# Optimization experiments

Measured on AMD Instinct MI355X. Metric: run time of the kernel, lower is better.

Reference implementation:

```python
import jax, jax.numpy as jnp
import numpy as np

VOCAB, H, L, B, T = 32000, 256, 10, 256, 512


def setup_inputs() -> dict:
    key = jax.random.key(0)
    ks = jax.random.split(key, 6)
    s = 1.0 / np.sqrt(H)
    return {
        "tokens": jax.random.randint(ks[0], (B, T), 0, VOCAB),
        "hidden0": jnp.zeros((L, B, H), jnp.float32),
        "emb": jax.random.normal(ks[1], (VOCAB, H), jnp.float32),
        "Wx_w": jax.random.normal(ks[2], (L, H, H), jnp.float32) * s,
        "Wx_b": jax.random.normal(ks[3], (L, H), jnp.float32) * s,
        "Wh_w": jax.random.normal(ks[4], (L, H, H), jnp.float32) * s,
        "Wh_b": jax.random.normal(ks[5], (L, H), jnp.float32) * s,
    }


def reference(tokens, hidden0, emb, Wx_w, Wx_b, Wh_w, Wh_b):
    # tokens: [B,T] int; hidden0: [L,B,H]; weights stacked over layers.
    embedded = emb[tokens]                    # [B,T,H]
    xs = jnp.swapaxes(embedded, 0, 1)         # [T,B,H]

    def time_step(h, x_t):                    # h: [L,B,H], x_t: [B,H]
        def layer_step(x, layer):
            wx, bx, wh, bh, hl = layer
            # torch Linear: y = x @ W.T + b
            new_h = jnp.tanh(x @ wx.T + bx + hl @ wh.T + bh)
            return new_h, new_h
        x_out, new_h = jax.lax.scan(layer_step, x_t, (Wx_w, Wx_b, Wh_w, Wh_b, h))
        return new_h, x_out                   # carry new hidden stack, emit top-layer output

    h_final, outs = jax.lax.scan(time_step, hidden0, xs)  # outs: [T,B,H]
    return jnp.swapaxes(outs, 0, 1), h_final  # ([B,T,H], [L,B,H])
```

## Files before the change

kernel.cpp:

```cpp
#include <hip/hip_runtime.h>

#define HDIM   256
#define NLAYER 10
#define BATCH  256
#define TSTEPS 512
#define NTHR   512
#define DEPTH  8
#define NREC   160
#define NFEED  16
#define NWG    176

typedef __attribute__((ext_vector_type(8))) short short8;
typedef __attribute__((ext_vector_type(4))) float f32x4;

__device__ __forceinline__ unsigned short bf16_rne(float f) {
    unsigned v = __float_as_uint(f);
    unsigned r = v + 0x7FFFu + ((v >> 16) & 1u);
    return (unsigned short)(r >> 16);
}
__device__ __forceinline__ float bf16_f(unsigned short b) {
    return __uint_as_float(((unsigned)b) << 16);
}
__device__ __forceinline__ float fast_tanh(float v) {
    float a = fabsf(v);
    float e = __expf(-2.0f * a);
    float r = (1.0f - e) / (1.0f + e);
    return __builtin_copysignf(r, v);
}
__device__ __forceinline__ void cvt8(const float* __restrict__ p, short8& hi, short8& lo) {
#pragma unroll
    for (int e = 0; e < 8; ++e) {
        float f = p[e];
        unsigned short h = bf16_rne(f);
        hi[e] = (short)h;
        lo[e] = (short)bf16_rne(f - bf16_f(h));
    }
}

#define MFMA16(a, b, c) __builtin_amdgcn_mfma_f32_16x16x32_bf16((a), (b), (c), 0, 0, 0)

__device__ __forceinline__ void wait_ge(int* f, int need) {
    while (__hip_atomic_load(f, __ATOMIC_RELAXED, __HIP_MEMORY_SCOPE_AGENT) < need)
        __builtin_amdgcn_s_sleep(1);
}
#define AT_LD(p)    __hip_atomic_load((p), __ATOMIC_RELAXED, __HIP_MEMORY_SCOPE_AGENT)
#define AT_ST(p, v) __hip_atomic_store((p), (v), __ATOMIC_RELAXED, __HIP_MEMORY_SCOPE_AGENT)
#define VMDRAIN()   asm volatile("s_waitcnt vmcnt(0)" ::: "memory")
#define PKF(a, b)   (((unsigned long long)__float_as_uint(b) << 32) | __float_as_uint(a))

#define WXH 0
#define HHI 131072
#define HLO 139264

__device__ __forceinline__ void stage_whi_f32(const float* __restrict__ src, char* smem, int tid) {
    for (int i = 0; i < 16; ++i) {
        const int ch = tid + i * NTHR;
        const int r = ch >> 5, kb = ch & 31;
        short8 hi, lo;
        cvt8(src + (size_t)r * HDIM + kb * 8, hi, lo);
        *(short8*)(smem + r * 512 + ((kb * 16) ^ ((r & 7) << 4))) = hi;
    }
}

__global__ void __launch_bounds__(NTHR) rnn_pipe(
    const int* __restrict__ tokens, const float* __restrict__ hidden0,
    const float* __restrict__ emb,
    const float* __restrict__ Wx_w, const float* __restrict__ Wx_b,
    const float* __restrict__ Wh_w, const float* __restrict__ Wh_b,
    float* __restrict__ u,
    int* __restrict__ fu,
    int* __restrict__ fd,
    float* __restrict__ out) {
    const int bid = blockIdx.x;
    const int tid = threadIdx.x;
    const int wv = tid >> 6;
    const int lane = tid & 63;
    const int ln15 = lane & 15;
    const int kq = (lane >> 4) << 3;
    const int hi16 = (lane >> 4) << 4;
    const int swz = (ln15 & 7) << 4;
    const int srow = tid >> 5;
    const int scb = tid & 31;

    __shared__ char smem[147456];
    float* hfinal = out + (size_t)BATCH * TSTEPS * HDIM;

    if (bid < NREC) {
        const int l = bid >> 4, s16 = bid & 15;
        const bool ship = (l < NLAYER - 1);

        if (ship) stage_whi_f32(Wx_w + (size_t)(l + 1) * 65536, smem, tid);
        short8 whh[2][8], whl[2][8], wxl[2][8];
        {
            const float* whsrc = Wh_w + (size_t)l * 65536;
            const float* wxsrc = Wx_w + (size_t)(l + 1) * 65536;
#define WINIT(ni, kc) do { \
            cvt8(whsrc + (size_t)(wv * 32 + ni * 16 + ln15) * HDIM + kc * 32 + kq, whh[ni][kc], whl[ni][kc]); \
            if (ship) { short8 _d; \
                cvt8(wxsrc + (size_t)(wv * 32 + ni * 16 + ln15) * HDIM + kc * 32 + kq, _d, wxl[ni][kc]); } \
            else { wxl[ni][kc] = short8{0,0,0,0,0,0,0,0}; } \
            asm volatile("" : "+v"(whh[ni][kc]), "+v"(whl[ni][kc]), "+v"(wxl[ni][kc])); \
        } while (0)
            WINIT(0,0); WINIT(0,1); WINIT(0,2); WINIT(0,3);
            WINIT(0,4); WINIT(0,5); WINIT(0,6); WINIT(0,7);
            WINIT(1,0); WINIT(1,1); WINIT(1,2); WINIT(1,3);
            WINIT(1,4); WINIT(1,5); WINIT(1,6); WINIT(1,7);
#undef WINIT
        }
        {
            short8 hi, lo;
            cvt8(hidden0 + ((size_t)(l * BATCH + s16 * 16 + srow)) * HDIM + scb * 8, hi, lo);
            const int so = srow * 512 + ((scb * 16) ^ ((srow & 7) << 4));
            *(short8*)(smem + HHI + so) = hi;
            *(short8*)(smem + HLO + so) = lo;
        }
        float bvn[2] = { 0.f, 0.f };
        if (ship) {
#pragma unroll
            for (int ni = 0; ni < 2; ++ni) {
                const int col = wv * 32 + ni * 16 + ln15;
                bvn[ni] = Wx_b[(l + 1) * HDIM + col] + Wh_b[(l + 1) * HDIM + col];
            }
        }

        int* fuMe = fu + ((size_t)l * 16 + s16) * TSTEPS;
        int* fuNx = ship ? fu + ((size_t)(l + 1) * 16 + s16) * TSTEPS : nullptr;
        int* fuG  = (l < NLAYER - 2) ? fu + ((size_t)(l + 2) * 16 + s16) * TSTEPS : nullptr;
        int* fdA  = fd + (size_t)s16 * TSTEPS;
        const unsigned long long* myu = (const unsigned long long*)
            (u + ((size_t)l * 16 + s16) * DEPTH * 4096);
        unsigned long long* nxu = ship ? (unsigned long long*)
            (u + ((size_t)(l + 1) * 16 + s16) * DEPTH * 4096) : nullptr;

        __syncthreads();

        for (int t = 0; t < TSTEPS; ++t) {
            if (tid == 0) wait_ge(fuMe + t, 1);
            if (tid == 64 && ship) {
                if (l < NLAYER - 2) { if (t >= 11) wait_ge(fuG + (t - 11), 1); }
                else                { if (t >= 9)  wait_ge(fdA + (t - 9), 1); }
            }
            __syncthreads();

            const unsigned long long* up = myu + (size_t)(t & 7) * 2048 + (size_t)tid * 4;
            unsigned long long q0 = AT_LD(up), q1 = AT_LD(up + 1),
                               q2 = AT_LD(up + 2), q3 = AT_LD(up + 3);

            const bool doU = ship && (t >= 1);
            f32x4 ah0a = {}, ah0b = {}, ah1a = {}, ah1b = {};
            f32x4 au0 = {}, au1 = {};
#define HX_KC(kc, A0, A1) do { \
            const int _off = ((kc) * 64 + hi16) ^ swz; \
            const short8 hh = *(const short8*)(smem + HHI + ln15 * 512 + _off); \
            const short8 hl = *(const short8*)(smem + HLO + ln15 * 512 + _off); \
            A0 = MFMA16(hh, whh[0][kc], A0);  A1 = MFMA16(hh, whh[1][kc], A1); \
            A0 = MFMA16(hh, whl[0][kc], A0);  A1 = MFMA16(hh, whl[1][kc], A1); \
            A0 = MFMA16(hl, whh[0][kc], A0);  A1 = MFMA16(hl, whh[1][kc], A1); \
            if (doU) { \
                const short8 bh0 = *(const short8*)(smem + WXH + (wv * 32 + ln15) * 512 + _off); \
                const short8 bh1 = *(const short8*)(smem + WXH + (wv * 32 + 16 + ln15) * 512 + _off); \
                au0 = MFMA16(hh, bh0, au0);         au1 = MFMA16(hh, bh1, au1); \
                au0 = MFMA16(hh, wxl[0][kc], au0);  au1 = MFMA16(hh, wxl[1][kc], au1); \
                au0 = MFMA16(hl, bh0, au0);         au1 = MFMA16(hl, bh1, au1); \
            } \
        } while (0)
            HX_KC(0, ah0a, ah1a); HX_KC(1, ah0a, ah1a);
            HX_KC(2, ah0a, ah1a); HX_KC(3, ah0a, ah1a);
            HX_KC(4, ah0b, ah1b); HX_KC(5, ah0b, ah1b);
            HX_KC(6, ah0b, ah1b); HX_KC(7, ah0b, ah1b);
#undef HX_KC

            VMDRAIN();
            __syncthreads();

            if (tid == 0) {
                if (ship && t >= 2) AT_ST(fuNx + (t - 2), 1);
                if (!ship) AT_ST(fdA + t, 1);
            }
            unsigned pk[2][4];
            {
                const float uv[2][4] = {
                    { __uint_as_float((unsigned)q0), __uint_as_float((unsigned)(q0 >> 32)),
                      __uint_as_float((unsigned)q1), __uint_as_float((unsigned)(q1 >> 32)) },
                    { __uint_as_float((unsigned)q2), __uint_as_float((unsigned)(q2 >> 32)),
                      __uint_as_float((unsigned)q3), __uint_as_float((unsigned)(q3 >> 32)) } };
#pragma unroll
                for (int r = 0; r < 4; ++r) {
                    const float y0 = fast_tanh(ah0a[r] + ah0b[r] + uv[0][r]);
                    const float y1 = fast_tanh(ah1a[r] + ah1b[r] + uv[1][r]);
                    unsigned short h0 = bf16_rne(y0), h1 = bf16_rne(y1);
                    pk[0][r] = (unsigned)h0 | ((unsigned)bf16_rne(y0 - bf16_f(h0)) << 16);
                    pk[1][r] = (unsigned)h1 | ((unsigned)bf16_rne(y1 - bf16_f(h1)) << 16);
                }
            }
#pragma unroll
            for (int ni = 0; ni < 2; ++ni) {
                const int col = wv * 32 + ni * 16 + ln15;
#pragma unroll
                for (int r = 0; r < 4; ++r) {
                    const int row = ((lane >> 4) << 2) + r;
                    const int so = row * 512 + ((2 * col) ^ ((row & 7) << 4));
                    *(unsigned short*)(smem + HHI + so) = (unsigned short)(pk[ni][r] & 0xffffu);
                    *(unsigned short*)(smem + HLO + so) = (unsigned short)(pk[ni][r] >> 16);
                    if (!ship) {
                        const float y = bf16_f((unsigned short)(pk[ni][r] & 0xffffu)) +
                                        bf16_f((unsigned short)(pk[ni][r] >> 16));
                        out[((size_t)(s16 * 16 + row) * TSTEPS + t) * HDIM + col] = y;
                    }
                    if (t == TSTEPS - 1) {
                        const float y = bf16_f((unsigned short)(pk[ni][r] & 0xffffu)) +
                                        bf16_f((unsigned short)(pk[ni][r] >> 16));
                        hfinal[((size_t)l * BATCH + s16 * 16 + row) * HDIM + col] = y;
                    }
                }
            }
            if (doU) {
                unsigned long long* us = nxu + (size_t)((t - 1) & 7) * 2048 + (size_t)tid * 4;
                AT_ST(us + 0, PKF(au0[0] + bvn[0], au0[1] + bvn[0]));
                AT_ST(us + 1, PKF(au0[2] + bvn[0], au0[3] + bvn[0]));
                AT_ST(us + 2, PKF(au1[0] + bvn[1], au1[1] + bvn[1]));
                AT_ST(us + 3, PKF(au1[2] + bvn[1], au1[3] + bvn[1]));
            }
        }

        if (ship) {
            if (tid == 64) {
                if (l < NLAYER - 2) wait_ge(fuG + 501, 1);
                else                wait_ge(fdA + 503, 1);
            }
            __syncthreads();
            f32x4 au0 = {}, au1 = {};
#define UE_KC(kc) do { \
            const int _off = ((kc) * 64 + hi16) ^ swz; \
            const short8 hh = *(const short8*)(smem + HHI + ln15 * 512 + _off); \
            const short8 hl = *(const short8*)(smem + HLO + ln15 * 512 + _off); \
            const short8 bh0 = *(const short8*)(smem + WXH + (wv * 32 + ln15) * 512 + _off); \
            const short8 bh1 = *(const short8*)(smem + WXH + (wv * 32 + 16 + ln15) * 512 + _off); \
            au0 = MFMA16(hh, bh0, au0);         au1 = MFMA16(hh, bh1, au1); \
            au0 = MFMA16(hh, wxl[0][kc], au0);  au1 = MFMA16(hh, wxl[1][kc], au1); \
            au0 = MFMA16(hl, bh0, au0);         au1 = MFMA16(hl, bh1, au1); \
        } while (0)
            UE_KC(0); UE_KC(1); UE_KC(2); UE_KC(3);
            UE_KC(4); UE_KC(5); UE_KC(6); UE_KC(7);
#undef UE_KC
            unsigned long long* us = nxu + (size_t)(511 & 7) * 2048 + (size_t)tid * 4;
            AT_ST(us + 0, PKF(au0[0] + bvn[0], au0[1] + bvn[0]));
            AT_ST(us + 1, PKF(au0[2] + bvn[0], au0[3] + bvn[0]));
            AT_ST(us + 2, PKF(au1[0] + bvn[1], au1[1] + bvn[1]));
            AT_ST(us + 3, PKF(au1[2] + bvn[1], au1[3] + bvn[1]));
            VMDRAIN();
            __syncthreads();
            if (tid == 0) {
                AT_ST(fuNx + 510, 1);
                AT_ST(fuNx + 511, 1);
            }
        }
    } else {
        const int s16 = bid - NREC;
        stage_whi_f32(Wx_w, smem, tid);
        short8 wxl[2][8];
#define FWINIT(ni, kc) do { \
        short8 _d; \
        cvt8(Wx_w + (size_t)(wv * 32 + ni * 16 + ln15) * HDIM + kc * 32 + kq, _d, wxl[ni][kc]); \
        asm volatile("" : "+v"(wxl[ni][kc])); \
    } while (0)
        FWINIT(0,0); FWINIT(0,1); FWINIT(0,2); FWINIT(0,3);
        FWINIT(0,4); FWINIT(0,5); FWINIT(0,6); FWINIT(0,7);
        FWINIT(1,0); FWINIT(1,1); FWINIT(1,2); FWINIT(1,3);
        FWINIT(1,4); FWINIT(1,5); FWINIT(1,6); FWINIT(1,7);
#undef FWINIT
        float b0[2];
#pragma unroll
        for (int ni = 0; ni < 2; ++ni) {
            const int col = wv * 32 + ni * 16 + ln15;
            b0[ni] = Wx_b[col] + Wh_b[col];
        }
        int* fuMe = fu + (size_t)s16 * TSTEPS;
        int* fuG  = fu + ((size_t)16 + s16) * TSTEPS;
        unsigned long long* nxu = (unsigned long long*)
            (u + (size_t)s16 * DEPTH * 4096);
        __syncthreads();

        for (int t = 0; t < TSTEPS; ++t) {
            if (tid == 0 && t >= 10) wait_ge(fuG + (t - 10), 1);
            __syncthreads();
            {
                const int tok = tokens[(s16 * 16 + srow) * TSTEPS + t];
                short8 hi, lo;
                cvt8(emb + (size_t)tok * HDIM + scb * 8, hi, lo);
                const int so = srow * 512 + ((scb * 16) ^ ((srow & 7) << 4));
                *(short8*)(smem + HHI + so) = hi;
                *(short8*)(smem + HLO + so) = lo;
            }
            __syncthreads();
            f32x4 ax0 = {}, ax1 = {};
#define FX_KC(kc) do { \
            const int _off = ((kc) * 64 + hi16) ^ swz; \
            const short8 xh = *(const short8*)(smem + HHI + ln15 * 512 + _off); \
            const short8 xl = *(const short8*)(smem + HLO + ln15 * 512 + _off); \
            const short8 bh0 = *(const short8*)(smem + WXH + (wv * 32 + ln15) * 512 + _off); \
            const short8 bh1 = *(const short8*)(smem + WXH + (wv * 32 + 16 + ln15) * 512 + _off); \
            ax0 = MFMA16(xh, bh0, ax0);         ax1 = MFMA16(xh, bh1, ax1); \
            ax0 = MFMA16(xh, wxl[0][kc], ax0);  ax1 = MFMA16(xh, wxl[1][kc], ax1); \
            ax0 = MFMA16(xl, bh0, ax0);         ax1 = MFMA16(xl, bh1, ax1); \
        } while (0)
            FX_KC(0); FX_KC(1); FX_KC(2); FX_KC(3);
            FX_KC(4); FX_KC(5); FX_KC(6); FX_KC(7);
#undef FX_KC
            unsigned long long* us = nxu + (size_t)(t & 7) * 2048 + (size_t)tid * 4;
            AT_ST(us + 0, PKF(ax0[0] + b0[0], ax0[1] + b0[0]));
            AT_ST(us + 1, PKF(ax0[2] + b0[0], ax0[3] + b0[0]));
            AT_ST(us + 2, PKF(ax1[0] + b0[1], ax1[1] + b0[1]));
            AT_ST(us + 3, PKF(ax1[2] + b0[1], ax1[3] + b0[1]));
            VMDRAIN();
            __syncthreads();
            if (tid == 0) AT_ST(fuMe + t, 1);
        }
    }
}

extern "C" void kernel_launch(void* const* d_in, const int* in_sizes, int n_in,
                              void* d_out, int out_size, void* d_ws, size_t ws_size,
                              hipStream_t stream) {
    const int* tokens = (const int*)d_in[0];
    const float* hidden0 = (const float*)d_in[1];
    const float* emb = (const float*)d_in[2];
    const float* Wx_w = (const float*)d_in[3];
    const float* Wx_b = (const float*)d_in[4];
    const float* Wh_w = (const float*)d_in[5];
    const float* Wh_b = (const float*)d_in[6];
    float* out = (float*)d_out;

    char* ws = (char*)d_ws;
    size_t off = 0;
    auto carve = [&](size_t bytes) -> void* {
        void* p = ws + off;
        off = (off + bytes + 255) & ~(size_t)255;
        return p;
    };
    float* u = (float*)carve((size_t)NLAYER * 16 * DEPTH * 4096 * 4);
    int* fu = (int*)carve((size_t)NLAYER * 16 * TSTEPS * 4);
    int* fd = (int*)carve((size_t)16 * TSTEPS * 4);
    (void)ws_size; (void)in_sizes; (void)n_in; (void)out_size;

    hipMemsetAsync(fu, 0, (size_t)(NLAYER * 16 + 16) * TSTEPS * 4, stream);

    void* args[] = { (void*)&tokens, (void*)&hidden0, (void*)&emb,
                     (void*)&Wx_w, (void*)&Wx_b, (void*)&Wh_w, (void*)&Wh_b,
                     (void*)&u, (void*)&fu, (void*)&fd, (void*)&out };
    hipLaunchCooperativeKernel((void*)rnn_pipe, dim3(NWG), dim3(NTHR), args, 0, stream);
}
```

Before: 3.372 ms.

## Remap workgroups by XCC and use cheaper non-atomic u transfers when same-XCC

Workgroups are reassigned so that, assuming round-robin XCC dispatch, each batch slice's feed and layer workgroups tend to land on the same XCC. Each workgroup records its hardware XCC id in a workspace table and, after a grid-wide arrival barrier, checks whether its producer and consumer share its XCC. For same-XCC pairs, the u handoff uses plain vector stores and sc0 dwordx4 loads instead of agent-scope 64-bit atomics, which aims to cut cross-XCC coherence latency on the recurrence's critical path. This depends on coherence within an XCC holding for sc0 loads together with the existing vmcnt drain and flags, and it adds a startup barrier.

```diff
diff --git a/kernel.cpp b/kernel.cpp
--- a/kernel.cpp
+++ b/kernel.cpp
@@ -6,12 +6,11 @@
 #define TSTEPS 512
 #define NTHR   512
 #define DEPTH  8
-#define NREC   160
-#define NFEED  16
 #define NWG    176
 
 typedef __attribute__((ext_vector_type(8))) short short8;
 typedef __attribute__((ext_vector_type(4))) float f32x4;
+typedef __attribute__((ext_vector_type(4))) unsigned u32x4;
 
 __device__ __forceinline__ unsigned short bf16_rne(float f) {
     unsigned v = __float_as_uint(f);
@@ -59,6 +58,25 @@
         short8 hi, lo;
         cvt8(src + (size_t)r * HDIM + kb * 8, hi, lo);
         *(short8*)(smem + r * 512 + ((kb * 16) ^ ((r & 7) << 4))) = hi;
+    }
+}
+
+__device__ __forceinline__ void u_store(char* us, bool loc,
+                                        const f32x4& a0, const f32x4& a1,
+                                        float b0, float b1) {
+    if (loc) {
+        u32x4 sa = { __float_as_uint(a0[0] + b0), __float_as_uint(a0[1] + b0),
+                     __float_as_uint(a0[2] + b0), __float_as_uint(a0[3] + b0) };
+        u32x4 sb = { __float_as_uint(a1[0] + b1), __float_as_uint(a1[1] + b1),
+                     __float_as_uint(a1[2] + b1), __float_as_uint(a1[3] + b1) };
+        *(u32x4*)us = sa;
+        *(u32x4*)(us + 16) = sb;
+    } else {
+        unsigned long long* q = (unsigned long long*)us;
+        AT_ST(q + 0, PKF(a0[0] + b0, a0[1] + b0));
+        AT_ST(q + 1, PKF(a0[2] + b0, a0[3] + b0));
+        AT_ST(q + 2, PKF(a1[0] + b1, a1[1] + b1));
+        AT_ST(q + 3, PKF(a1[2] + b1, a1[3] + b1));
     }
 }
 
@@ -70,6 +88,7 @@
     float* __restrict__ u,
     int* __restrict__ fu,
     int* __restrict__ fd,
+    int* __restrict__ xcct,
     float* __restrict__ out) {
     const int bid = blockIdx.x;
     const int tid = threadIdx.x;
@@ -82,11 +101,22 @@
     const int srow = tid >> 5;
     const int scb = tid & 31;
 
+    const int x8 = bid & 7, jj = bid >> 3, sh = jj / 11, lp = jj % 11;
+    const int s16 = x8 + (sh << 3);
+    const bool isFeed = (lp == 0);
+    const int l = lp - 1;
+
     __shared__ char smem[147456];
     float* hfinal = out + (size_t)BATCH * TSTEPS * HDIM;
 
-    if (bid < NREC) {
-        const int l = bid >> 4, s16 = bid & 15;
+    unsigned my_xcc;
+    asm volatile("s_getreg_b32 %0, hwreg(HW_REG_XCC_ID)" : "=s"(my_xcc));
+    if (tid == 0) {
+        AT_ST(xcct + bid, (int)my_xcc + 1);
+        __hip_atomic_fetch_add(xcct + 192, 1, __ATOMIC_RELEASE, __HIP_MEMORY_SCOPE_AGENT);
+    }
+
+    if (!isFeed) {
         const bool ship = (l < NLAYER - 1);
 
         if (ship) stage_whi_f32(Wx_w + (size_t)(l + 1) * 65536, smem, tid);
@@ -127,12 +157,15 @@
         int* fuNx = ship ? fu + ((size_t)(l + 1) * 16 + s16) * TSTEPS : nullptr;
         int* fuG  = (l < NLAYER - 2) ? fu + ((size_t)(l + 2) * 16 + s16) * TSTEPS : nullptr;
         int* fdA  = fd + (size_t)s16 * TSTEPS;
-        const unsigned long long* myu = (const unsigned long long*)
-            (u + ((size_t)l * 16 + s16) * DEPTH * 4096);
-        unsigned long long* nxu = ship ? (unsigned long long*)
-            (u + ((size_t)(l + 1) * 16 + s16) * DEPTH * 4096) : nullptr;
-
+        const char* myu = (const char*)(u + ((size_t)l * 16 + s16) * DEPTH * 4096);
+        char* nxu = ship ? (char*)(u + ((size_t)(l + 1) * 16 + s16) * DEPTH * 4096) : nullptr;
+
+        if (tid == 0) wait_ge(xcct + 192, NWG);
         __syncthreads();
+        const int pbid = x8 + 8 * (l + 11 * sh);
+        const int cbid = x8 + 8 * ((l + 2) + 11 * sh);
+        const bool locP = (AT_LD(xcct + pbid) == (int)my_xcc + 1);
+        const bool locC = ship ? (AT_LD(xcct + cbid) == (int)my_xcc + 1) : false;
 
         for (int t = 0; t < TSTEPS; ++t) {
             if (tid == 0) wait_ge(fuMe + t, 1);
@@ -142,9 +175,17 @@
             }
             __syncthreads();
 
-            const unsigned long long* up = myu + (size_t)(t & 7) * 2048 + (size_t)tid * 4;
-            unsigned long long q0 = AT_LD(up), q1 = AT_LD(up + 1),
-                               q2 = AT_LD(up + 2), q3 = AT_LD(up + 3);
+            u32x4 la = {}, lb = {};
+            unsigned long long q0 = 0, q1 = 0, q2 = 0, q3 = 0;
+            const char* up = myu + ((size_t)(t & 7) << 14) + ((size_t)tid << 5);
+            if (locP) {
+                asm volatile("global_load_dwordx4 %0, %2, off sc0\n\t"
+                             "global_load_dwordx4 %1, %2, off offset:16 sc0"
+                             : "=&v"(la), "=&v"(lb) : "v"(up) : "memory");
+            } else {
+                const unsigned long long* upq = (const unsigned long long*)up;
+                q0 = AT_LD(upq); q1 = AT_LD(upq + 1); q2 = AT_LD(upq + 2); q3 = AT_LD(upq + 3);
+            }
 
             const bool doU = ship && (t >= 1);
             f32x4 ah0a = {}, ah0b = {}, ah1a = {}, ah1b = {};
@@ -171,27 +212,33 @@
 #undef HX_KC
 
             VMDRAIN();
+            __builtin_amdgcn_sched_barrier(0);
             __syncthreads();
 
             if (tid == 0) {
                 if (ship && t >= 2) AT_ST(fuNx + (t - 2), 1);
                 if (!ship) AT_ST(fdA + t, 1);
             }
+            f32x4 uva, uvb;
+            if (locP) {
+                uva = f32x4{ __uint_as_float(la[0]), __uint_as_float(la[1]),
+                             __uint_as_float(la[2]), __uint_as_float(la[3]) };
+                uvb = f32x4{ __uint_as_float(lb[0]), __uint_as_float(lb[1]),
+                             __uint_as_float(lb[2]), __uint_as_float(lb[3]) };
+            } else {
+                uva = f32x4{ __uint_as_float((unsigned)q0), __uint_as_float((unsigned)(q0 >> 32)),
+                             __uint_as_float((unsigned)q1), __uint_as_float((unsigned)(q1 >> 32)) };
+                uvb = f32x4{ __uint_as_float((unsigned)q2), __uint_as_float((unsigned)(q2 >> 32)),
+                             __uint_as_float((unsigned)q3), __uint_as_float((unsigned)(q3 >> 32)) };
+            }
             unsigned pk[2][4];
-            {
-                const float uv[2][4] = {
-                    { __uint_as_float((unsigned)q0), __uint_as_float((unsigned)(q0 >> 32)),
-                      __uint_as_float((unsigned)q1), __uint_as_float((unsigned)(q1 >> 32)) },
-                    { __uint_as_float((unsigned)q2), __uint_as_float((unsigned)(q2 >> 32)),
-                      __uint_as_float((unsigned)q3), __uint_as_float((unsigned)(q3 >> 32)) } };
-#pragma unroll
-                for (int r = 0; r < 4; ++r) {
-                    const float y0 = fast_tanh(ah0a[r] + ah0b[r] + uv[0][r]);
-                    const float y1 = fast_tanh(ah1a[r] + ah1b[r] + uv[1][r]);
-                    unsigned short h0 = bf16_rne(y0), h1 = bf16_rne(y1);
-                    pk[0][r] = (unsigned)h0 | ((unsigned)bf16_rne(y0 - bf16_f(h0)) << 16);
-                    pk[1][r] = (unsigned)h1 | ((unsigned)bf16_rne(y1 - bf16_f(h1)) << 16);
-                }
+#pragma unroll
+            for (int r = 0; r < 4; ++r) {
+                const float y0 = fast_tanh(ah0a[r] + ah0b[r] + uva[r]);
+                const float y1 = fast_tanh(ah1a[r] + ah1b[r] + uvb[r]);
+                unsigned short h0 = bf16_rne(y0), h1 = bf16_rne(y1);
+                pk[0][r] = (unsigned)h0 | ((unsigned)bf16_rne(y0 - bf16_f(h0)) << 16);
+                pk[1][r] = (unsigned)h1 | ((unsigned)bf16_rne(y1 - bf16_f(h1)) << 16);
             }
 #pragma unroll
             for (int ni = 0; ni < 2; ++ni) {
@@ -214,13 +261,9 @@
                     }
                 }
             }
-            if (doU) {
-                unsigned long long* us = nxu + (size_t)((t - 1) & 7) * 2048 + (size_t)tid * 4;
-                AT_ST(us + 0, PKF(au0[0] + bvn[0], au0[1] + bvn[0]));
-                AT_ST(us + 1, PKF(au0[2] + bvn[0], au0[3] + bvn[0]));
-                AT_ST(us + 2, PKF(au1[0] + bvn[1], au1[1] + bvn[1]));
-                AT_ST(us + 3, PKF(au1[2] + bvn[1], au1[3] + bvn[1]));
-            }
+            if (doU)
+                u_store(nxu + ((size_t)((t - 1) & 7) << 14) + ((size_t)tid << 5),
+                        locC, au0, au1, bvn[0], bvn[1]);
         }
 
         if (ship) {
@@ -243,11 +286,8 @@
             UE_KC(0); UE_KC(1); UE_KC(2); UE_KC(3);
             UE_KC(4); UE_KC(5); UE_KC(6); UE_KC(7);
 #undef UE_KC
-            unsigned long long* us = nxu + (size_t)(511 & 7) * 2048 + (size_t)tid * 4;
-            AT_ST(us + 0, PKF(au0[0] + bvn[0], au0[1] + bvn[0]));
-            AT_ST(us + 1, PKF(au0[2] + bvn[0], au0[3] + bvn[0]));
-            AT_ST(us + 2, PKF(au1[0] + bvn[1], au1[1] + bvn[1]));
-            AT_ST(us + 3, PKF(au1[2] + bvn[1], au1[3] + bvn[1]));
+            u_store(nxu + ((size_t)(511 & 7) << 14) + ((size_t)tid << 5),
+                    locC, au0, au1, bvn[0], bvn[1]);
             VMDRAIN();
             __syncthreads();
             if (tid == 0) {
@@ -256,7 +296,6 @@
             }
         }
     } else {
-        const int s16 = bid - NREC;
         stage_whi_f32(Wx_w, smem, tid);
         short8 wxl[2][8];
 #define FWINIT(ni, kc) do { \
@@ -277,9 +316,12 @@
         }
         int* fuMe = fu + (size_t)s16 * TSTEPS;
         int* fuG  = fu + ((size_t)16 + s16) * TSTEPS;
-        unsigned long long* nxu = (unsigned long long*)
-            (u + (size_t)s16 * DEPTH * 4096);
+        char* nxu = (char*)(u + (size_t)s16 * DEPTH * 4096);
+
+        if (tid == 0) wait_ge(xcct + 192, NWG);
         __syncthreads();
+        const int cbid = x8 + 8 * (1 + 11 * sh);
+        const bool locC = (AT_LD(xcct + cbid) == (int)my_xcc + 1);
 
         for (int t = 0; t < TSTEPS; ++t) {
             if (tid == 0 && t >= 10) wait_ge(fuG + (t - 10), 1);
@@ -307,11 +349,8 @@
             FX_KC(0); FX_KC(1); FX_KC(2); FX_KC(3);
             FX_KC(4); FX_KC(5); FX_KC(6); FX_KC(7);
 #undef FX_KC
-            unsigned long long* us = nxu + (size_t)(t & 7) * 2048 + (size_t)tid * 4;
-            AT_ST(us + 0, PKF(ax0[0] + b0[0], ax0[1] + b0[0]));
-            AT_ST(us + 1, PKF(ax0[2] + b0[0], ax0[3] + b0[0]));
-            AT_ST(us + 2, PKF(ax1[0] + b0[1], ax1[1] + b0[1]));
-            AT_ST(us + 3, PKF(ax1[2] + b0[1], ax1[3] + b0[1]));
+            u_store(nxu + ((size_t)(t & 7) << 14) + ((size_t)tid << 5),
+                    locC, ax0, ax1, b0[0], b0[1]);
             VMDRAIN();
             __syncthreads();
             if (tid == 0) AT_ST(fuMe + t, 1);
@@ -341,12 +380,13 @@
     float* u = (float*)carve((size_t)NLAYER * 16 * DEPTH * 4096 * 4);
     int* fu = (int*)carve((size_t)NLAYER * 16 * TSTEPS * 4);
     int* fd = (int*)carve((size_t)16 * TSTEPS * 4);
+    int* xcct = (int*)carve(1024);
     (void)ws_size; (void)in_sizes; (void)n_in; (void)out_size;
 
-    hipMemsetAsync(fu, 0, (size_t)(NLAYER * 16 + 16) * TSTEPS * 4, stream);
+    hipMemsetAsync(fu, 0, (size_t)327680 + 32768 + 1024, stream);
 
     void* args[] = { (void*)&tokens, (void*)&hidden0, (void*)&emb,
                      (void*)&Wx_w, (void*)&Wx_b, (void*)&Wh_w, (void*)&Wh_b,
-                     (void*)&u, (void*)&fu, (void*)&fd, (void*)&out };
+                     (void*)&u, (void*)&fu, (void*)&fd, (void*)&xcct, (void*)&out };
     hipLaunchCooperativeKernel((void*)rnn_pipe, dim3(NWG), dim3(NTHR), args, 0, stream);
 }
```

Result: slower. 4.176 ms (+23.8%).

## Double-buffer hidden state in LDS to drop one barrier per recurrent step

Applied to the files above, without the earlier changes.

Gives the recurrent hidden state two ping-pong LDS buffers, so each step reads one buffer and writes the other. This removes the second __syncthreads per timestep. It also prefetches the next step's input projection from global memory during the current step's MFMAs and shifts the inter-layer flag signalling by one step to keep the ring buffer safe. Embedding loads and output stores become nontemporal. The cost is extra LDS use, tighter flag lag margins and a riskier synchronisation protocol.

```diff
diff --git a/kernel.cpp b/kernel.cpp
--- a/kernel.cpp
+++ b/kernel.cpp
@@ -7,7 +7,6 @@
 #define NTHR   512
 #define DEPTH  8
 #define NREC   160
-#define NFEED  16
 #define NWG    176
 
 typedef __attribute__((ext_vector_type(8))) short short8;
@@ -36,6 +35,15 @@
         lo[e] = (short)bf16_rne(f - bf16_f(h));
     }
 }
+__device__ __forceinline__ void cvt8_nt(const float* __restrict__ p, short8& hi, short8& lo) {
+#pragma unroll
+    for (int e = 0; e < 8; ++e) {
+        float f = __builtin_nontemporal_load(p + e);
+        unsigned short h = bf16_rne(f);
+        hi[e] = (short)h;
+        lo[e] = (short)bf16_rne(f - bf16_f(h));
+    }
+}
 
 #define MFMA16(a, b, c) __builtin_amdgcn_mfma_f32_16x16x32_bf16((a), (b), (c), 0, 0, 0)
 
@@ -49,8 +57,7 @@
 #define PKF(a, b)   (((unsigned long long)__float_as_uint(b) << 32) | __float_as_uint(a))
 
 #define WXH 0
-#define HHI 131072
-#define HLO 139264
+#define HPL 131072
 
 __device__ __forceinline__ void stage_whi_f32(const float* __restrict__ src, char* smem, int tid) {
     for (int i = 0; i < 16; ++i) {
@@ -82,7 +89,7 @@
     const int srow = tid >> 5;
     const int scb = tid & 31;
 
-    __shared__ char smem[147456];
+    __shared__ char smem[163840];
     float* hfinal = out + (size_t)BATCH * TSTEPS * HDIM;
 
     if (bid < NREC) {
@@ -111,8 +118,8 @@
             short8 hi, lo;
             cvt8(hidden0 + ((size_t)(l * BATCH + s16 * 16 + srow)) * HDIM + scb * 8, hi, lo);
             const int so = srow * 512 + ((scb * 16) ^ ((srow & 7) << 4));
-            *(short8*)(smem + HHI + so) = hi;
-            *(short8*)(smem + HLO + so) = lo;
+            *(short8*)(smem + HPL + so) = hi;
+            *(short8*)(smem + HPL + 8192 + so) = lo;
         }
         float bvn[2] = { 0.f, 0.f };
         if (ship) {
@@ -125,125 +132,146 @@
 
         int* fuMe = fu + ((size_t)l * 16 + s16) * TSTEPS;
         int* fuNx = ship ? fu + ((size_t)(l + 1) * 16 + s16) * TSTEPS : nullptr;
-        int* fuG  = (l < NLAYER - 2) ? fu + ((size_t)(l + 2) * 16 + s16) * TSTEPS : nullptr;
-        int* fdA  = fd + (size_t)s16 * TSTEPS;
+        int* fWit = (l <= 7) ? fu + ((size_t)(l + 2) * 16 + s16) * TSTEPS
+                             : fd + (size_t)s16 * TSTEPS;
+        int* fdMe = fd + (size_t)s16 * TSTEPS;
         const unsigned long long* myu = (const unsigned long long*)
-            (u + ((size_t)l * 16 + s16) * DEPTH * 4096);
+            (u + ((size_t)(l * 16 + s16)) * DEPTH * 4096);
         unsigned long long* nxu = ship ? (unsigned long long*)
-            (u + ((size_t)(l + 1) * 16 + s16) * DEPTH * 4096) : nullptr;
+            (u + ((size_t)((l + 1) * 16 + s16)) * DEPTH * 4096) : nullptr;
 
         __syncthreads();
-
-        for (int t = 0; t < TSTEPS; ++t) {
-            if (tid == 0) wait_ge(fuMe + t, 1);
-            if (tid == 64 && ship) {
-                if (l < NLAYER - 2) { if (t >= 11) wait_ge(fuG + (t - 11), 1); }
-                else                { if (t >= 9)  wait_ge(fdA + (t - 9), 1); }
-            }
-            __syncthreads();
-
-            const unsigned long long* up = myu + (size_t)(t & 7) * 2048 + (size_t)tid * 4;
-            unsigned long long q0 = AT_LD(up), q1 = AT_LD(up + 1),
-                               q2 = AT_LD(up + 2), q3 = AT_LD(up + 3);
-
-            const bool doU = ship && (t >= 1);
-            f32x4 ah0a = {}, ah0b = {}, ah1a = {}, ah1b = {};
-            f32x4 au0 = {}, au1 = {};
-#define HX_KC(kc, A0, A1) do { \
-            const int _off = ((kc) * 64 + hi16) ^ swz; \
-            const short8 hh = *(const short8*)(smem + HHI + ln15 * 512 + _off); \
-            const short8 hl = *(const short8*)(smem + HLO + ln15 * 512 + _off); \
-            A0 = MFMA16(hh, whh[0][kc], A0);  A1 = MFMA16(hh, whh[1][kc], A1); \
-            A0 = MFMA16(hh, whl[0][kc], A0);  A1 = MFMA16(hh, whl[1][kc], A1); \
-            A0 = MFMA16(hl, whh[0][kc], A0);  A1 = MFMA16(hl, whh[1][kc], A1); \
-            if (doU) { \
-                const short8 bh0 = *(const short8*)(smem + WXH + (wv * 32 + ln15) * 512 + _off); \
-                const short8 bh1 = *(const short8*)(smem + WXH + (wv * 32 + 16 + ln15) * 512 + _off); \
-                au0 = MFMA16(hh, bh0, au0);         au1 = MFMA16(hh, bh1, au1); \
-                au0 = MFMA16(hh, wxl[0][kc], au0);  au1 = MFMA16(hh, wxl[1][kc], au1); \
-                au0 = MFMA16(hl, bh0, au0);         au1 = MFMA16(hl, bh1, au1); \
-            } \
-        } while (0)
-            HX_KC(0, ah0a, ah1a); HX_KC(1, ah0a, ah1a);
-            HX_KC(2, ah0a, ah1a); HX_KC(3, ah0a, ah1a);
-            HX_KC(4, ah0b, ah1b); HX_KC(5, ah0b, ah1b);
-            HX_KC(6, ah0b, ah1b); HX_KC(7, ah0b, ah1b);
-#undef HX_KC
-
-            VMDRAIN();
-            __syncthreads();
-
-            if (tid == 0) {
-                if (ship && t >= 2) AT_ST(fuNx + (t - 2), 1);
-                if (!ship) AT_ST(fdA + t, 1);
-            }
-            unsigned pk[2][4];
-            {
-                const float uv[2][4] = {
-                    { __uint_as_float((unsigned)q0), __uint_as_float((unsigned)(q0 >> 32)),
-                      __uint_as_float((unsigned)q1), __uint_as_float((unsigned)(q1 >> 32)) },
-                    { __uint_as_float((unsigned)q2), __uint_as_float((unsigned)(q2 >> 32)),
-                      __uint_as_float((unsigned)q3), __uint_as_float((unsigned)(q3 >> 32)) } };
-#pragma unroll
-                for (int r = 0; r < 4; ++r) {
-                    const float y0 = fast_tanh(ah0a[r] + ah0b[r] + uv[0][r]);
-                    const float y1 = fast_tanh(ah1a[r] + ah1b[r] + uv[1][r]);
-                    unsigned short h0 = bf16_rne(y0), h1 = bf16_rne(y1);
-                    pk[0][r] = (unsigned)h0 | ((unsigned)bf16_rne(y0 - bf16_f(h0)) << 16);
-                    pk[1][r] = (unsigned)h1 | ((unsigned)bf16_rne(y1 - bf16_f(h1)) << 16);
-                }
-            }
-#pragma unroll
-            for (int ni = 0; ni < 2; ++ni) {
-                const int col = wv * 32 + ni * 16 + ln15;
-#pragma unroll
-                for (int r = 0; r < 4; ++r) {
-                    const int row = ((lane >> 4) << 2) + r;
-                    const int so = row * 512 + ((2 * col) ^ ((row & 7) << 4));
-                    *(unsigned short*)(smem + HHI + so) = (unsigned short)(pk[ni][r] & 0xffffu);
-                    *(unsigned short*)(smem + HLO + so) = (unsigned short)(pk[ni][r] >> 16);
-                    if (!ship) {
-                        const float y = bf16_f((unsigned short)(pk[ni][r] & 0xffffu)) +
-                                        bf16_f((unsigned short)(pk[ni][r] >> 16));
-                        out[((size_t)(s16 * 16 + row) * TSTEPS + t) * HDIM + col] = y;
-                    }
-                    if (t == TSTEPS - 1) {
-                        const float y = bf16_f((unsigned short)(pk[ni][r] & 0xffffu)) +
-                                        bf16_f((unsigned short)(pk[ni][r] >> 16));
-                        hfinal[((size_t)l * BATCH + s16 * 16 + row) * HDIM + col] = y;
-                    }
-                }
-            }
-            if (doU) {
-                unsigned long long* us = nxu + (size_t)((t - 1) & 7) * 2048 + (size_t)tid * 4;
-                AT_ST(us + 0, PKF(au0[0] + bvn[0], au0[1] + bvn[0]));
-                AT_ST(us + 1, PKF(au0[2] + bvn[0], au0[3] + bvn[0]));
-                AT_ST(us + 2, PKF(au1[0] + bvn[1], au1[1] + bvn[1]));
-                AT_ST(us + 3, PKF(au1[2] + bvn[1], au1[3] + bvn[1]));
-            }
-        }
-
-        if (ship) {
-            if (tid == 64) {
-                if (l < NLAYER - 2) wait_ge(fuG + 501, 1);
-                else                wait_ge(fdA + 503, 1);
-            }
-            __syncthreads();
-            f32x4 au0 = {}, au1 = {};
-#define UE_KC(kc) do { \
-            const int _off = ((kc) * 64 + hi16) ^ swz; \
-            const short8 hh = *(const short8*)(smem + HHI + ln15 * 512 + _off); \
-            const short8 hl = *(const short8*)(smem + HLO + ln15 * 512 + _off); \
+        if (tid == 0) wait_ge(fuMe + 0, 1);
+        __syncthreads();
+        unsigned long long qA0, qA1, qA2, qA3, qB0, qB1, qB2, qB3;
+        {
+            const unsigned long long* up = myu + (size_t)tid * 4;
+            qA0 = AT_LD(up); qA1 = AT_LD(up + 1); qA2 = AT_LD(up + 2); qA3 = AT_LD(up + 3);
+        }
+        qB0 = qB1 = qB2 = qB3 = 0;
+
+#define STEP(T, RDO, WRO, QC0, QC1, QC2, QC3, QN0, QN1, QN2, QN3) do {                    \
+        if (tid == 0 && (T) + 1 < TSTEPS) wait_ge(fuMe + (T) + 1, 1);                     \
+        if (tid == 64 && ship && (T) >= 9)                                                \
+            wait_ge(fWit + ((T) >= 11 ? (T) - 11 : 0), 1);                                \
+        __syncthreads();                                                                  \
+        asm volatile("" ::: "memory");                                                    \
+        if (tid == 0 && (T) >= 3) {                                                       \
+            if (ship) AT_ST(fuNx + (T) - 3, 1);                                           \
+            else      AT_ST(fdMe + (T) - 3, 1);                                           \
+        }                                                                                 \
+        VMDRAIN();                                                                        \
+        __builtin_amdgcn_sched_barrier(0);                                                \
+        if ((T) + 1 < TSTEPS) {                                                           \
+            const unsigned long long* up_ =                                               \
+                myu + (size_t)(((T) + 1) & 7) * 2048 + (size_t)tid * 4;                   \
+            QN0 = AT_LD(up_);     QN1 = AT_LD(up_ + 1);                                   \
+            QN2 = AT_LD(up_ + 2); QN3 = AT_LD(up_ + 3);                                   \
+        }                                                                                 \
+        const char* rdp = smem + HPL + (RDO);                                             \
+        char* wrp = smem + HPL + (WRO);                                                   \
+        const bool doU = ship && (T) >= 1;                                                \
+        f32x4 ah0a = {}, ah0b = {}, ah1a = {}, ah1b = {};                                 \
+        f32x4 au0 = {}, au1 = {};                                                         \
+        HX_KC(0, ah0a, ah1a); HX_KC(1, ah0a, ah1a);                                       \
+        HX_KC(2, ah0a, ah1a); HX_KC(3, ah0a, ah1a);                                       \
+        HX_KC(4, ah0b, ah1b); HX_KC(5, ah0b, ah1b);                                       \
+        HX_KC(6, ah0b, ah1b); HX_KC(7, ah0b, ah1b);                                       \
+        const f32x4 uva = { __uint_as_float((unsigned)(QC0)),                             \
+                            __uint_as_float((unsigned)((QC0) >> 32)),                     \
+                            __uint_as_float((unsigned)(QC1)),                             \
+                            __uint_as_float((unsigned)((QC1) >> 32)) };                   \
+        const f32x4 uvb = { __uint_as_float((unsigned)(QC2)),                             \
+                            __uint_as_float((unsigned)((QC2) >> 32)),                     \
+                            __uint_as_float((unsigned)(QC3)),                             \
+                            __uint_as_float((unsigned)((QC3) >> 32)) };                   \
+        unsigned pk[2][4];                                                                \
+        _Pragma("unroll")                                                                 \
+        for (int r = 0; r < 4; ++r) {                                                     \
+            const float y0 = fast_tanh(ah0a[r] + ah0b[r] + uva[r]);                       \
+            const float y1 = fast_tanh(ah1a[r] + ah1b[r] + uvb[r]);                       \
+            unsigned short h0 = bf16_rne(y0), h1 = bf16_rne(y1);                          \
+            pk[0][r] = (unsigned)h0 | ((unsigned)bf16_rne(y0 - bf16_f(h0)) << 16);        \
+            pk[1][r] = (unsigned)h1 | ((unsigned)bf16_rne(y1 - bf16_f(h1)) << 16);        \
+        }                                                                                 \
+        _Pragma("unroll")                                                                 \
+        for (int ni = 0; ni < 2; ++ni) {                                                  \
+            const int col = wv * 32 + ni * 16 + ln15;                                     \
+            _Pragma("unroll")                                                             \
+            for (int r = 0; r < 4; ++r) {                                                 \
+                const int row = ((lane >> 4) << 2) + r;                                   \
+                const int so = row * 512 + ((2 * col) ^ ((row & 7) << 4));                \
+                *(unsigned short*)(wrp + so) = (unsigned short)(pk[ni][r] & 0xffffu);     \
+                *(unsigned short*)(wrp + 8192 + so) = (unsigned short)(pk[ni][r] >> 16);  \
+                if (!ship) {                                                              \
+                    const float y = bf16_f((unsigned short)(pk[ni][r] & 0xffffu)) +       \
+                                    bf16_f((unsigned short)(pk[ni][r] >> 16));            \
+                    __builtin_nontemporal_store(                                          \
+                        y, out + ((size_t)(s16 * 16 + row) * TSTEPS + (T)) * HDIM + col); \
+                }                                                                         \
+                if ((T) == TSTEPS - 1) {                                                  \
+                    const float y = bf16_f((unsigned short)(pk[ni][r] & 0xffffu)) +       \
+                                    bf16_f((unsigned short)(pk[ni][r] >> 16));            \
+                    __builtin_nontemporal_store(                                          \
+                        y, hfinal + ((size_t)l * BATCH + s16 * 16 + row) * HDIM + col);   \
+                }                                                                         \
+            }                                                                             \
+        }                                                                                 \
+        if (doU) {                                                                        \
+            unsigned long long* us =                                                      \
+                nxu + (size_t)(((T) - 1) & 7) * 2048 + (size_t)tid * 4;                   \
+            AT_ST(us + 0, PKF(au0[0] + bvn[0], au0[1] + bvn[0]));                         \
+            AT_ST(us + 1, PKF(au0[2] + bvn[0], au0[3] + bvn[0]));                         \
+            AT_ST(us + 2, PKF(au1[0] + bvn[1], au1[1] + bvn[1]));                         \
+            AT_ST(us + 3, PKF(au1[2] + bvn[1], au1[3] + bvn[1]));                         \
+        }                                                                                 \
+    } while (0)
+
+#define HX_KC(kc, A0, A1) do {                                                            \
+        const int _off = ((kc) * 64 + hi16) ^ swz;                                        \
+        const short8 hh = *(const short8*)(rdp + ln15 * 512 + _off);                      \
+        const short8 hl = *(const short8*)(rdp + 8192 + ln15 * 512 + _off);               \
+        A0 = MFMA16(hh, whh[0][kc], A0);  A1 = MFMA16(hh, whh[1][kc], A1);                \
+        A0 = MFMA16(hh, whl[0][kc], A0);  A1 = MFMA16(hh, whl[1][kc], A1);                \
+        A0 = MFMA16(hl, whh[0][kc], A0);  A1 = MFMA16(hl, whh[1][kc], A1);                \
+        if (doU) {                                                                        \
             const short8 bh0 = *(const short8*)(smem + WXH + (wv * 32 + ln15) * 512 + _off); \
             const short8 bh1 = *(const short8*)(smem + WXH + (wv * 32 + 16 + ln15) * 512 + _off); \
-            au0 = MFMA16(hh, bh0, au0);         au1 = MFMA16(hh, bh1, au1); \
-            au0 = MFMA16(hh, wxl[0][kc], au0);  au1 = MFMA16(hh, wxl[1][kc], au1); \
-            au0 = MFMA16(hl, bh0, au0);         au1 = MFMA16(hl, bh1, au1); \
+            au0 = MFMA16(hh, bh0, au0);         au1 = MFMA16(hh, bh1, au1);               \
+            au0 = MFMA16(hh, wxl[0][kc], au0);  au1 = MFMA16(hh, wxl[1][kc], au1);        \
+            au0 = MFMA16(hl, bh0, au0);         au1 = MFMA16(hl, bh1, au1);               \
+        }                                                                                 \
+    } while (0)
+
+        for (int tb = 0; tb < TSTEPS / 2; ++tb) {
+            const int t0 = 2 * tb, t1 = 2 * tb + 1;
+            { STEP(t0, 0, 16384, qA0, qA1, qA2, qA3, qB0, qB1, qB2, qB3); }
+            { STEP(t1, 16384, 0, qB0, qB1, qB2, qB3, qA0, qA1, qA2, qA3); }
+        }
+#undef STEP
+
+        if (ship) {
+            if (tid == 64) wait_ge(fWit + 501, 1);
+            __syncthreads();
+            const char* rdp = smem + HPL;
+            f32x4 au0 = {}, au1 = {};
+            const bool doU = true;
+            HX_KC(0, au0, au1);
+            au0 = f32x4{}; au1 = f32x4{};
+#define UE_KC(kc) do {                                                                    \
+            const int _off = ((kc) * 64 + hi16) ^ swz;                                    \
+            const short8 hh = *(const short8*)(rdp + ln15 * 512 + _off);                  \
+            const short8 hl = *(const short8*)(rdp + 8192 + ln15 * 512 + _off);           \
+            const short8 bh0 = *(const short8*)(smem + WXH + (wv * 32 + ln15) * 512 + _off); \
+            const short8 bh1 = *(const short8*)(smem + WXH + (wv * 32 + 16 + ln15) * 512 + _off); \
+            au0 = MFMA16(hh, bh0, au0);         au1 = MFMA16(hh, bh1, au1);               \
+            au0 = MFMA16(hh, wxl[0][kc], au0);  au1 = MFMA16(hh, wxl[1][kc], au1);        \
+            au0 = MFMA16(hl, bh0, au0);         au1 = MFMA16(hl, bh1, au1);               \
         } while (0)
             UE_KC(0); UE_KC(1); UE_KC(2); UE_KC(3);
             UE_KC(4); UE_KC(5); UE_KC(6); UE_KC(7);
 #undef UE_KC
-            unsigned long long* us = nxu + (size_t)(511 & 7) * 2048 + (size_t)tid * 4;
+            unsigned long long* us = nxu + (size_t)7 * 2048 + (size_t)tid * 4;
             AT_ST(us + 0, PKF(au0[0] + bvn[0], au0[1] + bvn[0]));
             AT_ST(us + 1, PKF(au0[2] + bvn[0], au0[3] + bvn[0]));
             AT_ST(us + 2, PKF(au1[0] + bvn[1], au1[1] + bvn[1]));
@@ -251,10 +279,12 @@
             VMDRAIN();
             __syncthreads();
             if (tid == 0) {
+                AT_ST(fuNx + 509, 1);
                 AT_ST(fuNx + 510, 1);
                 AT_ST(fuNx + 511, 1);
             }
         }
+#undef HX_KC
     } else {
         const int s16 = bid - NREC;
         stage_whi_f32(Wx_w, smem, tid);
@@ -277,27 +307,26 @@
         }
         int* fuMe = fu + (size_t)s16 * TSTEPS;
         int* fuG  = fu + ((size_t)16 + s16) * TSTEPS;
-        unsigned long long* nxu = (unsigned long long*)
-            (u + (size_t)s16 * DEPTH * 4096);
+        unsigned long long* nxu = (unsigned long long*)(u + (size_t)s16 * DEPTH * 4096);
         __syncthreads();
 
         for (int t = 0; t < TSTEPS; ++t) {
-            if (tid == 0 && t >= 10) wait_ge(fuG + (t - 10), 1);
+            if (tid == 0 && t >= 8) wait_ge(fuG + (t >= 10 ? t - 10 : 0), 1);
             __syncthreads();
             {
                 const int tok = tokens[(s16 * 16 + srow) * TSTEPS + t];
                 short8 hi, lo;
-                cvt8(emb + (size_t)tok * HDIM + scb * 8, hi, lo);
+                cvt8_nt(emb + (size_t)tok * HDIM + scb * 8, hi, lo);
                 const int so = srow * 512 + ((scb * 16) ^ ((srow & 7) << 4));
-                *(short8*)(smem + HHI + so) = hi;
-                *(short8*)(smem + HLO + so) = lo;
+                *(short8*)(smem + HPL + so) = hi;
+                *(short8*)(smem + HPL + 8192 + so) = lo;
             }
             __syncthreads();
             f32x4 ax0 = {}, ax1 = {};
 #define FX_KC(kc) do { \
             const int _off = ((kc) * 64 + hi16) ^ swz; \
-            const short8 xh = *(const short8*)(smem + HHI + ln15 * 512 + _off); \
-            const short8 xl = *(const short8*)(smem + HLO + ln15 * 512 + _off); \
+            const short8 xh = *(const short8*)(smem + HPL + ln15 * 512 + _off); \
+            const short8 xl = *(const short8*)(smem + HPL + 8192 + ln15 * 512 + _off); \
             const short8 bh0 = *(const short8*)(smem + WXH + (wv * 32 + ln15) * 512 + _off); \
             const short8 bh1 = *(const short8*)(smem + WXH + (wv * 32 + 16 + ln15) * 512 + _off); \
             ax0 = MFMA16(xh, bh0, ax0);         ax1 = MFMA16(xh, bh1, ax1); \
@@ -343,7 +372,7 @@
     int* fd = (int*)carve((size_t)16 * TSTEPS * 4);
     (void)ws_size; (void)in_sizes; (void)n_in; (void)out_size;
 
-    hipMemsetAsync(fu, 0, (size_t)(NLAYER * 16 + 16) * TSTEPS * 4, stream);
+    hipMemsetAsync(fu, 0, (size_t)327680 + 32768, stream);
 
     void* args[] = { (void*)&tokens, (void*)&hidden0, (void*)&emb,
                      (void*)&Wx_w, (void*)&Wx_b, (void*)&Wh_w, (void*)&Wh_b,
```

After: 2.869 ms. 14.9% less time.
